# Optimization experiments

Hardware: AMD Instinct MI355X
Metric: run time of the kernel (lower is better)

Reference implementation:

```python
import jax, jax.numpy as jnp
import numpy as np


def setup_inputs() -> dict:
    key = jax.random.key(0)
    k1, k2, k3 = jax.random.split(key, 3)
    B, S, D_IN, D_OUT = 4, 2048, 4096, 4096
    x = jax.random.normal(k1, (B, S, D_IN), dtype=jnp.float32)
    # int8 quantized weight [out_features, in_features], values in [-127, 127]
    weight_q = jax.random.randint(k2, (D_OUT, D_IN), -127, 128, dtype=jnp.int32).astype(jnp.int8)
    # per-tensor symmetric scale, shape [1]
    scale = jax.random.uniform(k3, (1,), dtype=jnp.float32, minval=0.01, maxval=0.05)
    return {"x": x, "weight_q": weight_q, "scale": scale}


def reference(x, weight_q, scale):
    # scale_dequantize: upcast int8 weight to input dtype, multiply by scale
    w = weight_q.astype(x.dtype) * scale  # [out, in]
    # F.linear(input, weight): y = x @ w.T
    return jnp.einsum('bsi,oi->bso', x, w)
```

## Files before the change

kernel.cpp:

```cpp
#include <hip/hip_runtime.h>
#include <hip/hip_bf16.h>
#include <stdint.h>


#define M_DIM 8192
#define N_DIM 4096
#define K_DIM 4096
#define BM 256
#define BN 256
#define BK 64
#define NT (K_DIM / BK)

typedef __attribute__((ext_vector_type(4))) float    f32x4;
typedef __attribute__((ext_vector_type(4))) int      i32x4;
typedef __attribute__((ext_vector_type(2))) uint32_t u32x2;
typedef __attribute__((ext_vector_type(4))) uint32_t u32x4;
typedef __attribute__((ext_vector_type(8))) short    bf16x8;
typedef uint32_t u32;

__device__ __forceinline__ u32 fbits(float f) { return __builtin_bit_cast(u32, f); }
__device__ __forceinline__ u32 pack_bf16_trunc(float lo, float hi) {
    return __builtin_amdgcn_perm(fbits(hi), fbits(lo), 0x07060302u);
}
__device__ __forceinline__ int swzb(int row, int bytecol) {
    return row * 128 + (bytecol ^ ((row & 7) << 4));
}

__device__ __forceinline__ void gload_lds16(const void* g, void* s) {
    __builtin_amdgcn_global_load_lds(
        (const __attribute__((address_space(1))) void*)(uintptr_t)g,
        (__attribute__((address_space(3))) void*)(u32)(uintptr_t)s, 16, 0, 0);
}

#define WAIT_VM4()   do { asm volatile("s_waitcnt vmcnt(4)" ::: "memory");   \
                          __builtin_amdgcn_sched_barrier(0); } while (0)
#define WAIT_VM0()   do { asm volatile("s_waitcnt vmcnt(0)" ::: "memory");   \
                          __builtin_amdgcn_sched_barrier(0); } while (0)
#define BARRIER()    do { __builtin_amdgcn_s_barrier();                      \
                          __builtin_amdgcn_sched_barrier(0); } while (0)

__global__ __launch_bounds__(256)
void qlin_convert_w(const int* __restrict__ Wq, short* __restrict__ Wb)
{
    const size_t i = (size_t)blockIdx.x * 256 + threadIdx.x;
    i32x4 w0 = ((const i32x4*)Wq)[2 * i];
    i32x4 w1 = ((const i32x4*)Wq)[2 * i + 1];
    u32x4 q;
    q[0] = pack_bf16_trunc((float)w0[0], (float)w0[1]);
    q[1] = pack_bf16_trunc((float)w0[2], (float)w0[3]);
    q[2] = pack_bf16_trunc((float)w1[0], (float)w1[1]);
    q[3] = pack_bf16_trunc((float)w1[2], (float)w1[3]);
    ((u32x4*)Wb)[i] = q;
}

__global__ __launch_bounds__(256)
void qlin_convert_x(const float* __restrict__ X, short* __restrict__ Xb)
{
    const size_t i = (size_t)blockIdx.x * 256 + threadIdx.x;
    f32x4 a = ((const f32x4*)X)[2 * i];
    f32x4 b = ((const f32x4*)X)[2 * i + 1];
    u32x4 q;
    q[0] = pack_bf16_trunc(a[0], a[1]);
    q[1] = pack_bf16_trunc(a[2], a[3]);
    q[2] = pack_bf16_trunc(b[0], b[1]);
    q[3] = pack_bf16_trunc(b[2], b[3]);
    ((u32x4*)Xb)[i] = q;
}

__global__ __launch_bounds__(512, 2)
void qlin_gemm_p(const short* __restrict__ A, const short* __restrict__ B,
                 const float* __restrict__ scale_p, float* __restrict__ C)
{
    __shared__ __align__(16) char As[2][2][128 * 128];
    __shared__ __align__(16) char Bs[2][2][128 * 128];

    const int tid = threadIdx.x;
    const int nwg = (M_DIM / BM) * (N_DIM / BN);
    const int cpx = nwg / 8;
    const int bid = ((int)blockIdx.x % 8) * cpx + (int)blockIdx.x / 8;
    const int tileM = (bid / (N_DIM / BN)) * BM;
    const int tileN = (bid % (N_DIM / BN)) * BN;

    const int lane = tid & 63;
    const int wid  = tid >> 6;
    const int wr   = wid >> 2;
    const int wc   = wid & 3;
    const int lr   = lane & 15;
    const int lq   = lane >> 4;

    const int srow = lane >> 3;
    const int scol = ((lane & 7) ^ srow) << 4;
    const char* Ag = (const char*)A;
    const char* Bg = (const char*)B;

    auto stageA = [&](int buf, int h, int kt) {
#pragma unroll
        for (int j = 0; j < 2; ++j) {
            const int seg = wid * 2 + j;
            const char* src = Ag + (size_t)(tileM + h * 128 + seg * 8 + srow) * (K_DIM * 2)
                                 + kt * (BK * 2) + scol;
            gload_lds16(src, &As[buf][h][seg * 1024]);
        }
    };
    auto stageB = [&](int buf, int h, int kt) {
#pragma unroll
        for (int j = 0; j < 2; ++j) {
            const int seg = wid * 2 + j;
            const char* src = Bg + (size_t)(tileN + h * 128 + seg * 8 + srow) * (K_DIM * 2)
                                 + kt * (BK * 2) + scol;
            gload_lds16(src, &Bs[buf][h][seg * 1024]);
        }
    };

    f32x4  acc[8][4] = {};
    bf16x8 afr[4][2];
    bf16x8 b0fr[2][2], b2fr[2][2];

    auto swzh = [](int row, int bc) { return row * 128 + (bc ^ ((row & 7) << 4)); };
    auto ldA = [&](int buf, int mb) {
#pragma unroll
        for (int m = 0; m < 4; ++m) {
            const int row = (mb + m) * 16 + lr;
#pragma unroll
            for (int ks = 0; ks < 2; ++ks)
                afr[m][ks] = *(const bf16x8*)&As[buf][wr][swzh(row, ks * 64 + lq * 16)];
        }
    };
    auto ldB = [&](int buf, int nb, bf16x8 (&bf)[2][2]) {
#pragma unroll
        for (int n = 0; n < 2; ++n) {
            const int r = wc * 64 + (nb + n) * 16 + lr;
#pragma unroll
            for (int ks = 0; ks < 2; ++ks)
                bf[n][ks] = *(const bf16x8*)&Bs[buf][r >> 7][swzh(r & 127, ks * 64 + lq * 16)];
        }
    };
    auto quad = [&](int mb, int nb, bf16x8 (&bf)[2][2]) {
#pragma unroll
        for (int m = 0; m < 4; ++m)
#pragma unroll
            for (int n = 0; n < 2; ++n)
#pragma unroll
                for (int ks = 0; ks < 2; ++ks)
                    acc[mb + m][nb + n] = __builtin_amdgcn_mfma_f32_16x16x32_bf16(
                        afr[m][ks], bf[n][ks], acc[mb + m][nb + n], 0, 0, 0);
    };

    stageA(0, 0, 0); stageA(0, 1, 0);
    stageB(0, 0, 0); stageB(0, 1, 0);
    stageB(1, 0, 1); stageB(1, 1, 1);
    WAIT_VM4();
    BARRIER();

#pragma unroll 1
    for (int kt = 0; kt < NT; ++kt) {
        const int cur = kt & 1, nxt = cur ^ 1;

        ldA(cur, 0);
        ldB(cur, 0, b0fr);
        ldB(cur, 2, b2fr);
        if (kt + 1 < NT) { stageA(nxt, 0, kt + 1); stageA(nxt, 1, kt + 1); }

        __builtin_amdgcn_s_setprio(1);
        quad(0, 0, b0fr);
        quad(0, 2, b2fr);
        __builtin_amdgcn_s_setprio(0);

        ldA(cur, 4);

        BARRIER();
        if (kt + 2 < NT) { stageB(cur, 0, kt + 2); stageB(cur, 1, kt + 2); }

        __builtin_amdgcn_s_setprio(1);
        quad(4, 2, b2fr);
        quad(4, 0, b0fr);
        __builtin_amdgcn_s_setprio(0);

        if (kt + 2 < NT)      { WAIT_VM4(); }
        else if (kt + 1 < NT) { WAIT_VM0(); }
        BARRIER();
    }

    const float scl = scale_p[0];
#pragma unroll
    for (int m = 0; m < 8; ++m) {
        const int gm0 = tileM + wr * 128 + m * 16 + lq * 4;
#pragma unroll
        for (int n = 0; n < 4; ++n) {
            const int gn = tileN + wc * 64 + n * 16 + lr;
            float* cp = C + (size_t)gm0 * N_DIM + gn;
#pragma unroll
            for (int r = 0; r < 4; ++r)
                cp[(size_t)r * N_DIM] = acc[m][n][r] * scl;
        }
    }
}

#define TILE_BYTES (BM * BK * 2)
__global__ __launch_bounds__(512, 2)
void qlin_gemm8(const void* __restrict__ Asrc, const void* __restrict__ Bsrc,
                const float* __restrict__ scale_p, float* __restrict__ C)
{
    __shared__ char As[2 * TILE_BYTES];
    __shared__ char Bs[2 * TILE_BYTES];

    const int tid = threadIdx.x;
    const int nwg = (M_DIM / BM) * (N_DIM / BN);
    const int cpx = nwg / 8;
    const int bid = ((int)blockIdx.x % 8) * cpx + (int)blockIdx.x / 8;
    const int tileM = (bid / (N_DIM / BN)) * BM;
    const int tileN = (bid % (N_DIM / BN)) * BN;

    const int lane = tid & 63;
    const int wid  = tid >> 6;
    const int wr   = wid >> 2;
    const int wc   = wid & 3;
    const int lr   = lane & 15;
    const int lq   = lane >> 4;

    f32x4  aF[8]; i32x4 wF[8];

    const float* ag0 = (const float*)Asrc + (size_t)(tileM + (tid >> 4)) * K_DIM + (tid & 15) * 4;
    const int*   bg0 = (const int*)Bsrc  + (size_t)(tileN + (tid >> 4)) * K_DIM + (tid & 15) * 4;

    auto stage_load = [&](int kt) {
#pragma unroll
        for (int i = 0; i < 8; ++i)
            aF[i] = *(const f32x4*)(ag0 + (size_t)(32 * i) * K_DIM + kt * BK);
#pragma unroll
        for (int i = 0; i < 8; ++i)
            wF[i] = *(const i32x4*)(bg0 + (size_t)(32 * i) * K_DIM + kt * BK);
    };
    auto stage_writeA = [&](int nxt) {
        char* dst = As + nxt * TILE_BYTES;
#pragma unroll
        for (int i = 0; i < 8; ++i) {
            u32x2 p;
            p[0] = pack_bf16_trunc(aF[i][0], aF[i][1]);
            p[1] = pack_bf16_trunc(aF[i][2], aF[i][3]);
            *(u32x2*)(dst + swzb((tid >> 4) + 32 * i, (tid & 15) * 8)) = p;
        }
    };
    auto stage_writeB = [&](int nxt) {
        char* dst = Bs + nxt * TILE_BYTES;
#pragma unroll
        for (int i = 0; i < 8; ++i) {
            u32x2 p;
            p[0] = pack_bf16_trunc((float)wF[i][0], (float)wF[i][1]);
            p[1] = pack_bf16_trunc((float)wF[i][2], (float)wF[i][3]);
            *(u32x2*)(dst + swzb((tid >> 4) + 32 * i, (tid & 15) * 8)) = p;
        }
    };

    f32x4  acc[8][4] = {};
    bf16x8 afr[4][2], bfr[2][2];

    auto ldA = [&](const char* buf, int mb) {
#pragma unroll
        for (int m = 0; m < 4; ++m) {
            const int row = wr * 128 + (mb + m) * 16 + lr;
#pragma unroll
            for (int ks = 0; ks < 2; ++ks)
                afr[m][ks] = *(const bf16x8*)(buf + swzb(row, ks * 64 + lq * 16));
        }
    };
    auto ldB = [&](const char* buf, int nb) {
#pragma unroll
        for (int n = 0; n < 2; ++n) {
            const int row = wc * 64 + (nb + n) * 16 + lr;
#pragma unroll
            for (int ks = 0; ks < 2; ++ks)
                bfr[n][ks] = *(const bf16x8*)(buf + swzb(row, ks * 64 + lq * 16));
        }
    };
    auto quad = [&](int mb, int nb) {
        __builtin_amdgcn_s_setprio(1);
#pragma unroll
        for (int m = 0; m < 4; ++m)
#pragma unroll
            for (int n = 0; n < 2; ++n)
#pragma unroll
                for (int ks = 0; ks < 2; ++ks)
                    acc[mb + m][nb + n] = __builtin_amdgcn_mfma_f32_16x16x32_bf16(
                        afr[m][ks], bfr[n][ks], acc[mb + m][nb + n], 0, 0, 0);
        __builtin_amdgcn_s_setprio(0);
    };

    stage_load(0);
    stage_writeA(0);
    stage_writeB(0);
    __syncthreads();

#pragma unroll 1
    for (int kt = 0; kt < NT; ++kt) {
        const int cur = kt & 1, nxt = cur ^ 1;
        const bool more = (kt + 1) < NT;
        const char* Ab = As + cur * TILE_BYTES;
        const char* Bb = Bs + cur * TILE_BYTES;

        if (more) stage_load(kt + 1);

        ldA(Ab, 0); ldB(Bb, 0); quad(0, 0);
        ldB(Bb, 2);             quad(0, 2);
        ldA(Ab, 4);
        if (more) stage_writeA(nxt);
        quad(4, 2);
        ldB(Bb, 0);
        if (more) stage_writeB(nxt);
        quad(4, 0);

        __syncthreads();
    }

    const float scl = scale_p[0];
#pragma unroll
    for (int m = 0; m < 8; ++m) {
        const int gm0 = tileM + wr * 128 + m * 16 + lq * 4;
#pragma unroll
        for (int n = 0; n < 4; ++n) {
            const int gn = tileN + wc * 64 + n * 16 + lr;
            float* cp = C + (size_t)gm0 * N_DIM + gn;
#pragma unroll
            for (int r = 0; r < 4; ++r)
                cp[(size_t)r * N_DIM] = acc[m][n][r] * scl;
        }
    }
}

extern "C" void kernel_launch(void* const* d_in, const int* in_sizes, int n_in,
                              void* d_out, int out_size, void* d_ws, size_t ws_size,
                              hipStream_t stream)
{
    (void)in_sizes; (void)n_in; (void)out_size;
    const float* X     = (const float*)d_in[0];
    const int*   Wq    = (const int*)d_in[1];
    const float* scale = (const float*)d_in[2];
    float* C = (float*)d_out;

    const dim3 gblock(256);
    const dim3 ggrid((M_DIM / BM) * (N_DIM / BN));
    const size_t xbytes = (size_t)M_DIM * K_DIM * sizeof(short);
    const size_t wbytes = (size_t)N_DIM * K_DIM * sizeof(short);

    if (ws_size >= xbytes + wbytes) {
        short* Xb = (short*)d_ws;
        short* Wb = (short*)((char*)d_ws + xbytes);
        qlin_convert_x<<<dim3((size_t)M_DIM * K_DIM / (8 * 256)), gblock, 0, stream>>>(X, Xb);
        qlin_convert_w<<<dim3((size_t)N_DIM * K_DIM / (8 * 256)), gblock, 0, stream>>>(Wq, Wb);
        qlin_gemm_p<<<ggrid, dim3(512), 0, stream>>>(Xb, Wb, scale, C);
    } else {
        qlin_gemm8<<<ggrid, dim3(512), 0, stream>>>(X, Wq, scale, C);
    }
}
```

Before: 268.8 us.

## Software-pipeline second-half MFMAs across k-iterations with separate A fragment buffers

Splits the A fragment registers into two sets so the second half of the MFMA work for tile k is deferred into iteration k+1. There it overlaps with issuing the next A stage loads and the LDS reads for the current tile. An explicit lgkmcnt wait is added before the barrier, and an epilogue finishes the last deferred quads. This is meant to hide LDS read latency and barrier stalls behind matrix work. The cost is an extra 8 bf16x8 registers, which raises VGPR pressure.

```diff
diff --git a/kernel.cpp b/kernel.cpp
--- a/kernel.cpp
+++ b/kernel.cpp
@@ -32,6 +32,8 @@
         (__attribute__((address_space(3))) void*)(u32)(uintptr_t)s, 16, 0, 0);
 }
 
+#define WAIT_LGKM0() do { asm volatile("s_waitcnt lgkmcnt(0)" ::: "memory"); \
+                          __builtin_amdgcn_sched_barrier(0); } while (0)
 #define WAIT_VM4()   do { asm volatile("s_waitcnt vmcnt(4)" ::: "memory");   \
                           __builtin_amdgcn_sched_barrier(0); } while (0)
 #define WAIT_VM0()   do { asm volatile("s_waitcnt vmcnt(0)" ::: "memory");   \
@@ -113,17 +115,17 @@
     };
 
     f32x4  acc[8][4] = {};
-    bf16x8 afr[4][2];
+    bf16x8 afr0[4][2], afr4[4][2];
     bf16x8 b0fr[2][2], b2fr[2][2];
 
     auto swzh = [](int row, int bc) { return row * 128 + (bc ^ ((row & 7) << 4)); };
-    auto ldA = [&](int buf, int mb) {
+    auto ldA = [&](int buf, int mb, bf16x8 (&af)[4][2]) {
 #pragma unroll
         for (int m = 0; m < 4; ++m) {
             const int row = (mb + m) * 16 + lr;
 #pragma unroll
             for (int ks = 0; ks < 2; ++ks)
-                afr[m][ks] = *(const bf16x8*)&As[buf][wr][swzh(row, ks * 64 + lq * 16)];
+                af[m][ks] = *(const bf16x8*)&As[buf][wr][swzh(row, ks * 64 + lq * 16)];
         }
     };
     auto ldB = [&](int buf, int nb, bf16x8 (&bf)[2][2]) {
@@ -135,7 +137,8 @@
                 bf[n][ks] = *(const bf16x8*)&Bs[buf][r >> 7][swzh(r & 127, ks * 64 + lq * 16)];
         }
     };
-    auto quad = [&](int mb, int nb, bf16x8 (&bf)[2][2]) {
+    auto quad = [&](int mb, int nb, bf16x8 (&af)[4][2], bf16x8 (&bf)[2][2]) {
+        __builtin_amdgcn_s_setprio(1);
 #pragma unroll
         for (int m = 0; m < 4; ++m)
 #pragma unroll
@@ -143,7 +146,8 @@
 #pragma unroll
                 for (int ks = 0; ks < 2; ++ks)
                     acc[mb + m][nb + n] = __builtin_amdgcn_mfma_f32_16x16x32_bf16(
-                        afr[m][ks], bf[n][ks], acc[mb + m][nb + n], 0, 0, 0);
+                        af[m][ks], bf[n][ks], acc[mb + m][nb + n], 0, 0, 0);
+        __builtin_amdgcn_s_setprio(0);
     };
 
     stageA(0, 0, 0); stageA(0, 1, 0);
@@ -156,30 +160,32 @@
     for (int kt = 0; kt < NT; ++kt) {
         const int cur = kt & 1, nxt = cur ^ 1;
 
-        ldA(cur, 0);
+        if (kt + 1 < NT) { stageA(nxt, 0, kt + 1); stageA(nxt, 1, kt + 1); }
+
+        if (kt) {
+            quad(4, 2, afr4, b2fr);
+            quad(4, 0, afr4, b0fr);
+        }
+
+        ldA(cur, 0, afr0);
         ldB(cur, 0, b0fr);
         ldB(cur, 2, b2fr);
-        if (kt + 1 < NT) { stageA(nxt, 0, kt + 1); stageA(nxt, 1, kt + 1); }
-
-        __builtin_amdgcn_s_setprio(1);
-        quad(0, 0, b0fr);
-        quad(0, 2, b2fr);
-        __builtin_amdgcn_s_setprio(0);
-
-        ldA(cur, 4);
-
+        ldA(cur, 4, afr4);
+
+        quad(0, 0, afr0, b0fr);
+        quad(0, 2, afr0, b2fr);
+
+        WAIT_LGKM0();
         BARRIER();
         if (kt + 2 < NT) { stageB(cur, 0, kt + 2); stageB(cur, 1, kt + 2); }
-
-        __builtin_amdgcn_s_setprio(1);
-        quad(4, 2, b2fr);
-        quad(4, 0, b0fr);
-        __builtin_amdgcn_s_setprio(0);
 
         if (kt + 2 < NT)      { WAIT_VM4(); }
         else if (kt + 1 < NT) { WAIT_VM0(); }
         BARRIER();
     }
+
+    quad(4, 2, afr4, b2fr);
+    quad(4, 0, afr4, b0fr);
 
     const float scl = scale_p[0];
 #pragma unroll
```

Result: slower. 277.3 us (+3.2%).

## Load B fragments directly from global into registers, dropping LDS staging for B

Applied to the files above, without the earlier changes.

B tiles no longer go through shared memory. Each wave loads its own B fragments straight from global into registers, double-buffered two k-steps ahead, and the loop is unrolled by two to alternate the register sets. This cuts LDS capacity and traffic for B and removes one barrier per iteration. In exchange it costs more VGPRs, issues uncoalesced 16-byte global loads that waves sharing B columns duplicate, and exposes the kernel to global latency if the two-step prefetch is too short.

```diff
diff --git a/kernel.cpp b/kernel.cpp
--- a/kernel.cpp
+++ b/kernel.cpp
@@ -32,7 +32,7 @@
         (__attribute__((address_space(3))) void*)(u32)(uintptr_t)s, 16, 0, 0);
 }
 
-#define WAIT_VM4()   do { asm volatile("s_waitcnt vmcnt(4)" ::: "memory");   \
+#define WAIT_VM8()   do { asm volatile("s_waitcnt vmcnt(8)" ::: "memory");   \
                           __builtin_amdgcn_sched_barrier(0); } while (0)
 #define WAIT_VM0()   do { asm volatile("s_waitcnt vmcnt(0)" ::: "memory");   \
                           __builtin_amdgcn_sched_barrier(0); } while (0)
@@ -72,7 +72,6 @@
                  const float* __restrict__ scale_p, float* __restrict__ C)
 {
     __shared__ __align__(16) char As[2][2][128 * 128];
-    __shared__ __align__(16) char Bs[2][2][128 * 128];
 
     const int tid = threadIdx.x;
     const int nwg = (M_DIM / BM) * (N_DIM / BN);
@@ -102,19 +101,20 @@
             gload_lds16(src, &As[buf][h][seg * 1024]);
         }
     };
-    auto stageB = [&](int buf, int h, int kt) {
-#pragma unroll
-        for (int j = 0; j < 2; ++j) {
-            const int seg = wid * 2 + j;
-            const char* src = Bg + (size_t)(tileN + h * 128 + seg * 8 + srow) * (K_DIM * 2)
-                                 + kt * (BK * 2) + scol;
-            gload_lds16(src, &Bs[buf][h][seg * 1024]);
-        }
+
+    const char* bbase = Bg + (size_t)(tileN + wc * 64 + lr) * (K_DIM * 2) + lq * 16;
+    auto ldBg = [&](bf16x8 (&bf)[4][2], int kt) {
+#pragma unroll
+        for (int nb = 0; nb < 4; ++nb)
+#pragma unroll
+            for (int ks = 0; ks < 2; ++ks)
+                bf[nb][ks] = *(const bf16x8*)(bbase + (size_t)(nb * 16) * (K_DIM * 2)
+                                              + kt * (BK * 2) + ks * 64);
     };
 
     f32x4  acc[8][4] = {};
     bf16x8 afr[4][2];
-    bf16x8 b0fr[2][2], b2fr[2][2];
+    bf16x8 bP[4][2], bQ[4][2];
 
     auto swzh = [](int row, int bc) { return row * 128 + (bc ^ ((row & 7) << 4)); };
     auto ldA = [&](int buf, int mb) {
@@ -126,59 +126,43 @@
                 afr[m][ks] = *(const bf16x8*)&As[buf][wr][swzh(row, ks * 64 + lq * 16)];
         }
     };
-    auto ldB = [&](int buf, int nb, bf16x8 (&bf)[2][2]) {
-#pragma unroll
-        for (int n = 0; n < 2; ++n) {
-            const int r = wc * 64 + (nb + n) * 16 + lr;
-#pragma unroll
-            for (int ks = 0; ks < 2; ++ks)
-                bf[n][ks] = *(const bf16x8*)&Bs[buf][r >> 7][swzh(r & 127, ks * 64 + lq * 16)];
-        }
-    };
-    auto quad = [&](int mb, int nb, bf16x8 (&bf)[2][2]) {
-#pragma unroll
-        for (int m = 0; m < 4; ++m)
-#pragma unroll
-            for (int n = 0; n < 2; ++n)
-#pragma unroll
-                for (int ks = 0; ks < 2; ++ks)
-                    acc[mb + m][nb + n] = __builtin_amdgcn_mfma_f32_16x16x32_bf16(
-                        afr[m][ks], bf[n][ks], acc[mb + m][nb + n], 0, 0, 0);
+    auto quadrow = [&](int mb, bf16x8 (&bf)[4][2]) {
+        __builtin_amdgcn_s_setprio(1);
+#pragma unroll
+        for (int ks = 0; ks < 2; ++ks)
+#pragma unroll
+            for (int m = 0; m < 4; ++m)
+#pragma unroll
+                for (int nb = 0; nb < 4; ++nb)
+                    acc[mb + m][nb] = __builtin_amdgcn_mfma_f32_16x16x32_bf16(
+                        afr[m][ks], bf[nb][ks], acc[mb + m][nb], 0, 0, 0);
+        __builtin_amdgcn_s_setprio(0);
     };
 
     stageA(0, 0, 0); stageA(0, 1, 0);
-    stageB(0, 0, 0); stageB(0, 1, 0);
-    stageB(1, 0, 1); stageB(1, 1, 1);
-    WAIT_VM4();
+    ldBg(bP, 0);
+    ldBg(bQ, 1);
+    WAIT_VM8();
     BARRIER();
 
-#pragma unroll 1
-    for (int kt = 0; kt < NT; ++kt) {
-        const int cur = kt & 1, nxt = cur ^ 1;
+    auto body = [&](int kt, int cur, bf16x8 (&bCur)[4][2]) {
+        const int nxt = cur ^ 1;
+        if (kt + 1 < NT) { stageA(nxt, 0, kt + 1); stageA(nxt, 1, kt + 1); }
 
         ldA(cur, 0);
-        ldB(cur, 0, b0fr);
-        ldB(cur, 2, b2fr);
-        if (kt + 1 < NT) { stageA(nxt, 0, kt + 1); stageA(nxt, 1, kt + 1); }
-
-        __builtin_amdgcn_s_setprio(1);
-        quad(0, 0, b0fr);
-        quad(0, 2, b2fr);
-        __builtin_amdgcn_s_setprio(0);
-
+        quadrow(0, bCur);
         ldA(cur, 4);
-
-        BARRIER();
-        if (kt + 2 < NT) { stageB(cur, 0, kt + 2); stageB(cur, 1, kt + 2); }
-
-        __builtin_amdgcn_s_setprio(1);
-        quad(4, 2, b2fr);
-        quad(4, 0, b0fr);
-        __builtin_amdgcn_s_setprio(0);
-
-        if (kt + 2 < NT)      { WAIT_VM4(); }
+        quadrow(4, bCur);
+
+        if (kt + 2 < NT) { ldBg(bCur, kt + 2); WAIT_VM8(); }
         else if (kt + 1 < NT) { WAIT_VM0(); }
         BARRIER();
+    };
+
+#pragma unroll 1
+    for (int kt = 0; kt < NT; kt += 2) {
+        body(kt,     0, bP);
+        body(kt + 1, 1, bQ);
     }
 
     const float scl = scale_p[0];
```

Result: slower. 467.9 us (+74.1%).

## Switch bf16 GEMM inner loop to 32x32x16 MFMA with reordered LDS fragment loads

Applied to the files above, without the earlier changes.

Replaces the 16x16x32 bf16 MFMA tiling with 32x32x16 MFMA tiles. Each wave now computes a 4x2 grid of 32x32 accumulators, and the LDS fragment loads are re-indexed to match. Loading B once per k-tile and reusing it across all A sub-blocks is meant to cut LDS read traffic and instruction count. The schedule also changes: the next-A prefetch is issued before the fragment reads, and the epilogue row mapping is updated for the 32x32 output layout. In exchange, per-lane fragment register pressure rises, and the store pattern is less coalesced.

```diff
diff --git a/kernel.cpp b/kernel.cpp
--- a/kernel.cpp
+++ b/kernel.cpp
@@ -11,11 +11,12 @@
 #define BK 64
 #define NT (K_DIM / BK)
 
-typedef __attribute__((ext_vector_type(4))) float    f32x4;
-typedef __attribute__((ext_vector_type(4))) int      i32x4;
-typedef __attribute__((ext_vector_type(2))) uint32_t u32x2;
-typedef __attribute__((ext_vector_type(4))) uint32_t u32x4;
-typedef __attribute__((ext_vector_type(8))) short    bf16x8;
+typedef __attribute__((ext_vector_type(4)))  float    f32x4;
+typedef __attribute__((ext_vector_type(16))) float    f32x16;
+typedef __attribute__((ext_vector_type(4)))  int      i32x4;
+typedef __attribute__((ext_vector_type(2)))  uint32_t u32x2;
+typedef __attribute__((ext_vector_type(4)))  uint32_t u32x4;
+typedef __attribute__((ext_vector_type(8)))  short    bf16x8;
 typedef uint32_t u32;
 
 __device__ __forceinline__ u32 fbits(float f) { return __builtin_bit_cast(u32, f); }
@@ -85,8 +86,8 @@
     const int wid  = tid >> 6;
     const int wr   = wid >> 2;
     const int wc   = wid & 3;
-    const int lr   = lane & 15;
-    const int lq   = lane >> 4;
+    const int l31  = lane & 31;
+    const int lh   = lane >> 5;
 
     const int srow = lane >> 3;
     const int scol = ((lane & 7) ^ srow) << 4;
@@ -112,38 +113,40 @@
         }
     };
 
-    f32x4  acc[8][4] = {};
-    bf16x8 afr[4][2];
-    bf16x8 b0fr[2][2], b2fr[2][2];
+    f32x16 acc[4][2] = {};
+    bf16x8 amA[2][4], amB[2][4];
+    bf16x8 bn[2][4];
 
     auto swzh = [](int row, int bc) { return row * 128 + (bc ^ ((row & 7) << 4)); };
-    auto ldA = [&](int buf, int mb) {
-#pragma unroll
-        for (int m = 0; m < 4; ++m) {
-            const int row = (mb + m) * 16 + lr;
-#pragma unroll
-            for (int ks = 0; ks < 2; ++ks)
-                afr[m][ks] = *(const bf16x8*)&As[buf][wr][swzh(row, ks * 64 + lq * 16)];
-        }
-    };
-    auto ldB = [&](int buf, int nb, bf16x8 (&bf)[2][2]) {
-#pragma unroll
-        for (int n = 0; n < 2; ++n) {
-            const int r = wc * 64 + (nb + n) * 16 + lr;
-#pragma unroll
-            for (int ks = 0; ks < 2; ++ks)
-                bf[n][ks] = *(const bf16x8*)&Bs[buf][r >> 7][swzh(r & 127, ks * 64 + lq * 16)];
-        }
-    };
-    auto quad = [&](int mb, int nb, bf16x8 (&bf)[2][2]) {
-#pragma unroll
-        for (int m = 0; m < 4; ++m)
-#pragma unroll
-            for (int n = 0; n < 2; ++n)
-#pragma unroll
-                for (int ks = 0; ks < 2; ++ks)
-                    acc[mb + m][nb + n] = __builtin_amdgcn_mfma_f32_16x16x32_bf16(
-                        afr[m][ks], bf[n][ks], acc[mb + m][nb + n], 0, 0, 0);
+    auto ldA32 = [&](int buf, int mlo, bf16x8 (&am)[2][4]) {
+#pragma unroll
+        for (int mi = 0; mi < 2; ++mi) {
+            const int row = (mlo + mi) * 32 + l31;
+#pragma unroll
+            for (int ks = 0; ks < 4; ++ks)
+                am[mi][ks] = *(const bf16x8*)&As[buf][wr][swzh(row, ks * 32 + lh * 16)];
+        }
+    };
+    auto ldB32 = [&](int buf) {
+#pragma unroll
+        for (int ni = 0; ni < 2; ++ni) {
+            const int r = wc * 64 + ni * 32 + l31;
+#pragma unroll
+            for (int ks = 0; ks < 4; ++ks)
+                bn[ni][ks] = *(const bf16x8*)&Bs[buf][r >> 7][swzh(r & 127, ks * 32 + lh * 16)];
+        }
+    };
+    auto cluster = [&](int mlo, bf16x8 (&am)[2][4]) {
+        __builtin_amdgcn_s_setprio(1);
+#pragma unroll
+        for (int ks = 0; ks < 4; ++ks)
+#pragma unroll
+            for (int mi = 0; mi < 2; ++mi)
+#pragma unroll
+                for (int ni = 0; ni < 2; ++ni)
+                    acc[mlo + mi][ni] = __builtin_amdgcn_mfma_f32_32x32x16_bf16(
+                        am[mi][ks], bn[ni][ks], acc[mlo + mi][ni], 0, 0, 0);
+        __builtin_amdgcn_s_setprio(0);
     };
 
     stageA(0, 0, 0); stageA(0, 1, 0);
@@ -156,25 +159,17 @@
     for (int kt = 0; kt < NT; ++kt) {
         const int cur = kt & 1, nxt = cur ^ 1;
 
-        ldA(cur, 0);
-        ldB(cur, 0, b0fr);
-        ldB(cur, 2, b2fr);
         if (kt + 1 < NT) { stageA(nxt, 0, kt + 1); stageA(nxt, 1, kt + 1); }
 
-        __builtin_amdgcn_s_setprio(1);
-        quad(0, 0, b0fr);
-        quad(0, 2, b2fr);
-        __builtin_amdgcn_s_setprio(0);
-
-        ldA(cur, 4);
+        ldA32(cur, 0, amA);
+        ldB32(cur);
+        cluster(0, amA);
+        ldA32(cur, 2, amB);
 
         BARRIER();
         if (kt + 2 < NT) { stageB(cur, 0, kt + 2); stageB(cur, 1, kt + 2); }
 
-        __builtin_amdgcn_s_setprio(1);
-        quad(4, 2, b2fr);
-        quad(4, 0, b0fr);
-        __builtin_amdgcn_s_setprio(0);
+        cluster(2, amB);
 
         if (kt + 2 < NT)      { WAIT_VM4(); }
         else if (kt + 1 < NT) { WAIT_VM0(); }
@@ -183,17 +178,17 @@
 
     const float scl = scale_p[0];
 #pragma unroll
-    for (int m = 0; m < 8; ++m) {
-        const int gm0 = tileM + wr * 128 + m * 16 + lq * 4;
-#pragma unroll
-        for (int n = 0; n < 4; ++n) {
-            const int gn = tileN + wc * 64 + n * 16 + lr;
-            float* cp = C + (size_t)gm0 * N_DIM + gn;
-#pragma unroll
-            for (int r = 0; r < 4; ++r)
-                cp[(size_t)r * N_DIM] = acc[m][n][r] * scl;
-        }
-    }
+    for (int mi = 0; mi < 4; ++mi)
+#pragma unroll
+        for (int ni = 0; ni < 2; ++ni) {
+            const int gcol = tileN + wc * 64 + ni * 32 + l31;
+#pragma unroll
+            for (int r = 0; r < 16; ++r) {
+                const int grow = tileM + wr * 128 + mi * 32
+                               + (r & 3) + 8 * (r >> 2) + 4 * lh;
+                C[(size_t)grow * N_DIM + gcol] = acc[mi][ni][r] * scl;
+            }
+        }
 }
 
 #define TILE_BYTES (BM * BK * 2)
```

New measurement: 303.0 us. +12.7%, slower.
